# Optimization experiments

Hardware: AMD Instinct MI355X
Metric: run time of the kernel (lower is better)

## Reference

```python
import jax, jax.numpy as jnp
import numpy as np

DIM_Q = 1024
DIM_K = 1024
DIM_V = 1024


def setup_inputs() -> dict:
    key = jax.random.key(0)
    kx, kq, kk, kv = jax.random.split(key, 4)
    x = jax.random.normal(kx, (4, 2048, DIM_Q), dtype=jnp.float32)
    # torch nn.Linear weights: [out_features, in_features], y = x @ W.T
    scale = 1.0 / np.sqrt(DIM_Q)
    Wq = jax.random.uniform(kq, (DIM_K, DIM_Q), dtype=jnp.float32, minval=-scale, maxval=scale)
    Wk = jax.random.uniform(kk, (DIM_K, DIM_Q), dtype=jnp.float32, minval=-scale, maxval=scale)
    Wv = jax.random.uniform(kv, (DIM_V, DIM_Q), dtype=jnp.float32, minval=-scale, maxval=scale)
    return {"x": x, "Wq": Wq, "Wk": Wk, "Wv": Wv}


def reference(x, Wq, Wk, Wv):
    # q, k: [b, s, dim_k]; v: [b, s, dim_v]
    q = jnp.einsum('bsd,kd->bsk', x, Wq)
    k = jnp.einsum('bsd,kd->bsk', x, Wk)
    v = jnp.einsum('bsd,vd->bsv', x, Wv)
    norm_fact = 1.0 / jnp.sqrt(jnp.asarray(DIM_K, dtype=x.dtype))
    score = jnp.einsum('bik,bjk->bij', q, k) * norm_fact  # [b, s, s]
    score = jax.nn.softmax(score, axis=-1)
    att = jnp.einsum('bij,bjv->biv', score, v)
    att = att + v  # is_residual=True
    return att
```

## Files before the change

kernel.cpp:

```cpp
#include <hip/hip_runtime.h>
#include <hip/hip_bf16.h>

using bf16 = __hip_bfloat16;
typedef __attribute__((ext_vector_type(8))) short short8;
typedef __attribute__((ext_vector_type(4))) float floatx4;
typedef __attribute__((ext_vector_type(8))) int int8v;

__device__ __forceinline__ void async_ld16(const void* g, void* l) {
  __builtin_amdgcn_global_load_lds((const __attribute__((address_space(1))) void*)g,
                                   (__attribute__((address_space(3))) void*)l, 16, 0, 0);
}

__device__ __forceinline__ int pk4_fp8(float a, float b, float c, float d) {
  int v = __builtin_amdgcn_cvt_pk_fp8_f32(a, b, 0, false);
  return __builtin_amdgcn_cvt_pk_fp8_f32(c, d, v, true);
}

__device__ __forceinline__ int8v ld_frag16(const unsigned char* lo, const unsigned char* hi) {
  int4 l0 = *(const int4*)lo, h0 = *(const int4*)hi;
  int8v v;
  v[0] = l0.x; v[1] = l0.y; v[2] = l0.z; v[3] = l0.w;
  v[4] = h0.x; v[5] = h0.y; v[6] = h0.z; v[7] = h0.w;
  return v;
}


__device__ __forceinline__ void gemm_core(const bf16* __restrict__ At,
                                          const bf16* __restrict__ Bt,
                                          int K, bf16* lA, bf16* lB,
                                          floatx4 acc[4][4]) {
  const int tid  = threadIdx.x;
  const int w    = tid >> 6;
  const int lane = tid & 63;
  const int subM = (w >> 1) * 64;
  const int subN = (w & 1) * 64;
  const int fr   = lane & 15;
  const int fq   = lane >> 4;

  int srow[4], scol[4], sdst[4];
#pragma unroll
  for (int q = 0; q < 4; ++q) {
    int p = q * 256 + w * 64 + lane;
    int r = p >> 3;
    int j = (p & 7) ^ (r & 7);
    srow[q] = r;
    scol[q] = j * 8;
    sdst[q] = (q * 256 + w * 64) * 8;
  }
  int offA[2][4], offB[2][4];
#pragma unroll
  for (int kc = 0; kc < 2; ++kc)
#pragma unroll
    for (int i = 0; i < 4; ++i) {
      int rA = subM + i * 16 + fr;
      offA[kc][i] = (rA * 8 + ((kc * 4 + fq) ^ (rA & 7))) * 8;
      int rB = subN + i * 16 + fr;
      offB[kc][i] = (rB * 8 + ((kc * 4 + fq) ^ (rB & 7))) * 8;
    }

  floatx4 zero = {0.f, 0.f, 0.f, 0.f};
#pragma unroll
  for (int i = 0; i < 4; ++i)
#pragma unroll
    for (int j = 0; j < 4; ++j) acc[i][j] = zero;

  for (int k0 = 0; k0 < K; k0 += 64) {
    __syncthreads();
#pragma unroll
    for (int q = 0; q < 4; ++q) {
      async_ld16(At + (size_t)srow[q] * K + k0 + scol[q], lA + sdst[q]);
      async_ld16(Bt + (size_t)srow[q] * K + k0 + scol[q], lB + sdst[q]);
    }
    __syncthreads();
#pragma unroll
    for (int kc = 0; kc < 2; ++kc) {
      short8 a[4], b[4];
#pragma unroll
      for (int i = 0; i < 4; ++i) a[i] = *(const short8*)(lA + offA[kc][i]);
#pragma unroll
      for (int j = 0; j < 4; ++j) b[j] = *(const short8*)(lB + offB[kc][j]);
#pragma unroll
      for (int i = 0; i < 4; ++i)
#pragma unroll
        for (int j = 0; j < 4; ++j)
          acc[i][j] = __builtin_amdgcn_mfma_f32_16x16x32_bf16(a[i], b[j], acc[i][j], 0, 0, 0);
    }
  }
}

__device__ __forceinline__ void gemm_core_f8(const unsigned char* __restrict__ At,
                                             const unsigned char* __restrict__ Bt,
                                             int K, unsigned char* lA, unsigned char* lB,
                                             floatx4 acc[4][4]) {
  const int tid  = threadIdx.x;
  const int w    = tid >> 6;
  const int lane = tid & 63;
  const int subM = (w >> 1) * 64;
  const int subN = (w & 1) * 64;
  const int fr   = lane & 15;
  const int fq   = lane >> 4;

  int srow[4], scol[4], sdst[4];
#pragma unroll
  for (int q = 0; q < 4; ++q) {
    int p = q * 256 + w * 64 + lane;
    int r = p >> 3;
    int j = (p & 7) ^ (r & 7) ^ ((r & 8) >> 1);
    srow[q] = r;
    scol[q] = j * 16;
    sdst[q] = (q * 256 + w * 64) * 16;
  }
  int offA[2][4], offB[2][4];
#pragma unroll
  for (int h = 0; h < 2; ++h)
#pragma unroll
    for (int i = 0; i < 4; ++i) {
      int rA = subM + i * 16 + fr;
      offA[h][i] = rA * 128 + (((fq * 2 + h) ^ (rA & 7) ^ ((rA & 8) >> 1)) * 16);
      int rB = subN + i * 16 + fr;
      offB[h][i] = rB * 128 + (((fq * 2 + h) ^ (rB & 7) ^ ((rB & 8) >> 1)) * 16);
    }

  floatx4 zero = {0.f, 0.f, 0.f, 0.f};
#pragma unroll
  for (int i = 0; i < 4; ++i)
#pragma unroll
    for (int j = 0; j < 4; ++j) acc[i][j] = zero;

  for (int k0 = 0; k0 < K; k0 += 128) {
    __syncthreads();
#pragma unroll
    for (int q = 0; q < 4; ++q) {
      async_ld16(At + (size_t)srow[q] * K + k0 + scol[q], lA + sdst[q]);
      async_ld16(Bt + (size_t)srow[q] * K + k0 + scol[q], lB + sdst[q]);
    }
    __syncthreads();
    int8v a[4], b[4];
#pragma unroll
    for (int i = 0; i < 4; ++i) a[i] = ld_frag16(lA + offA[0][i], lA + offA[1][i]);
#pragma unroll
    for (int j = 0; j < 4; ++j) b[j] = ld_frag16(lB + offB[0][j], lB + offB[1][j]);
#pragma unroll
    for (int i = 0; i < 4; ++i)
#pragma unroll
      for (int j = 0; j < 4; ++j)
        acc[i][j] = __builtin_amdgcn_mfma_scale_f32_16x16x128_f8f6f4(
            a[i], b[j], acc[i][j], 0, 0, 0, 0x7F7F7F7F, 0, 0x7F7F7F7F);
  }
}

__device__ __forceinline__ void gemm_core_f8_v2(const unsigned char* __restrict__ At,
                                                const unsigned char* __restrict__ Bt,
                                                int K, unsigned char* lA, unsigned char* lB,
                                                floatx4 acc[4][8]) {
  const int tid  = threadIdx.x;
  const int w    = tid >> 6;
  const int lane = tid & 63;
  const int subM = (w >> 1) * 64;
  const int subN = (w & 1) * 128;
  const int fr   = lane & 15;
  const int fq   = lane >> 4;

  int srowA[4], scolA[4], sdstA[4];
#pragma unroll
  for (int q = 0; q < 4; ++q) {
    int p = q * 256 + w * 64 + lane;
    int r = p >> 3;
    int j = (p & 7) ^ (r & 7) ^ ((r & 8) >> 1);
    srowA[q] = r; scolA[q] = j * 16; sdstA[q] = (q * 256 + w * 64) * 16;
  }
  int srowB[8], scolB[8], sdstB[8];
#pragma unroll
  for (int q = 0; q < 8; ++q) {
    int p = q * 256 + w * 64 + lane;
    int r = p >> 3;
    int j = (p & 7) ^ (r & 7) ^ ((r & 8) >> 1);
    srowB[q] = r; scolB[q] = j * 16; sdstB[q] = (q * 256 + w * 64) * 16;
  }
  int offA[2][4], offB[2][8];
#pragma unroll
  for (int h = 0; h < 2; ++h) {
#pragma unroll
    for (int i = 0; i < 4; ++i) {
      int rA = subM + i * 16 + fr;
      offA[h][i] = rA * 128 + (((fq * 2 + h) ^ (rA & 7) ^ ((rA & 8) >> 1)) * 16);
    }
#pragma unroll
    for (int j = 0; j < 8; ++j) {
      int rB = subN + j * 16 + fr;
      offB[h][j] = rB * 128 + (((fq * 2 + h) ^ (rB & 7) ^ ((rB & 8) >> 1)) * 16);
    }
  }

  floatx4 zero = {0.f, 0.f, 0.f, 0.f};
#pragma unroll
  for (int i = 0; i < 4; ++i)
#pragma unroll
    for (int j = 0; j < 8; ++j) acc[i][j] = zero;

  for (int k0 = 0; k0 < K; k0 += 128) {
    __syncthreads();
#pragma unroll
    for (int q = 0; q < 4; ++q)
      async_ld16(At + (size_t)srowA[q] * K + k0 + scolA[q], lA + sdstA[q]);
#pragma unroll
    for (int q = 0; q < 8; ++q)
      async_ld16(Bt + (size_t)srowB[q] * K + k0 + scolB[q], lB + sdstB[q]);
    __syncthreads();
    int8v a[4];
#pragma unroll
    for (int i = 0; i < 4; ++i) a[i] = ld_frag16(lA + offA[0][i], lA + offA[1][i]);
#pragma unroll
    for (int j = 0; j < 8; ++j) {
      int8v bf = ld_frag16(lB + offB[0][j], lB + offB[1][j]);
#pragma unroll
      for (int i = 0; i < 4; ++i)
        acc[i][j] = __builtin_amdgcn_mfma_scale_f32_16x16x128_f8f6f4(
            a[i], bf, acc[i][j], 0, 0, 0, 0x7F7F7F7F, 0, 0x7F7F7F7F);
    }
  }
}

__global__ __launch_bounds__(256, 2) void proj_gemm(
    const bf16* __restrict__ Xbf, const bf16* __restrict__ Wvbf, bf16* __restrict__ Vbf,
    const unsigned char* __restrict__ X8, const unsigned char* __restrict__ Wq8,
    const unsigned char* __restrict__ Wk8,
    unsigned char* __restrict__ Qf8, unsigned char* __restrict__ Kf8) {
  __shared__ __align__(16) char lds[49152];
  const int id = blockIdx.x;
  const int tid = threadIdx.x, w = tid >> 6, lane = tid & 63;
  const int fr = lane & 15, fq = lane >> 4;

  if (id < 512) {
    const int r = id & 7, g = id >> 3;
    const int ty = r * 8 + (g & 7), tx = g >> 3;
    bf16* lA = (bf16*)lds;
    bf16* lB = (bf16*)(lds + 16384);
    floatx4 acc[4][4];
    gemm_core(Xbf + (size_t)ty * 128 * 1024, Wvbf + (size_t)tx * 128 * 1024,
              1024, lA, lB, acc);
    const int subM = (w >> 1) * 64, subN = (w & 1) * 64;
    const int rowBase = ty * 128 + subM;
    const int colBase = tx * 128 + subN;
#pragma unroll
    for (int i = 0; i < 4; ++i)
#pragma unroll
      for (int j = 0; j < 4; ++j)
#pragma unroll
        for (int rr = 0; rr < 4; ++rr) {
          int row = rowBase + i * 16 + fq * 4 + rr;
          int col = colBase + j * 16 + fr;
          Vbf[(size_t)row * 1024 + col] = __float2bfloat16(acc[i][j][rr]);
        }
  } else {
    const int local = id - 512;
    const int z = local >> 8, lid = local & 255;
    const int r = lid & 7, g = lid >> 3;
    const int ty = r * 8 + (g & 7);
    const int tx = g >> 3;
    unsigned char* lA = (unsigned char*)lds;
    unsigned char* lB = (unsigned char*)(lds + 16384);
    floatx4 acc[4][8];
    gemm_core_f8_v2(X8 + (size_t)ty * 128 * 1024,
                    (z == 0 ? Wq8 : Wk8) + (size_t)tx * 256 * 1024, 1024, lA, lB, acc);
    unsigned char* dst = (z == 0) ? Qf8 : Kf8;
    const int subM = (w >> 1) * 64, subN = (w & 1) * 128;
    const int rowBase = ty * 128 + subM;
    const int colBase = tx * 256 + subN;
#pragma unroll
    for (int i = 0; i < 4; ++i)
#pragma unroll
      for (int rr = 0; rr < 4; ++rr) {
        int row = rowBase + i * 16 + fq * 4 + rr;
        unsigned int p0 = (unsigned int)pk4_fp8(acc[i][0][rr], acc[i][1][rr],
                                                acc[i][2][rr], acc[i][3][rr]);
        unsigned int p1 = (unsigned int)pk4_fp8(acc[i][4][rr], acc[i][5][rr],
                                                acc[i][6][rr], acc[i][7][rr]);
        *(unsigned int*)&dst[(size_t)row * 1024 + colBase + fr * 4] = p0;
        *(unsigned int*)&dst[(size_t)row * 1024 + colBase + 64 + fr * 4] = p1;
      }
  }
}

__global__ __launch_bounds__(256, 2) void mid_kernel(
    const unsigned char* __restrict__ Qf8, const unsigned char* __restrict__ Kf8,
    unsigned char* __restrict__ S8, float* __restrict__ l,
    const bf16* __restrict__ Vbf, unsigned char* __restrict__ Vt8) {
  __shared__ __align__(16) char lds[49152];
  const int id = blockIdx.x;
  const int t = threadIdx.x;

  if (id < 512) {
    const int r = id & 7, g = id >> 3;
    const int b = g >> 4;
    const int rem = g & 15;
    const int ty = r * 2 + (rem & 1);
    const int tx = rem >> 1;
    unsigned char* lA = (unsigned char*)lds;
    unsigned char* lB = (unsigned char*)(lds + 16384);
    floatx4 acc[4][8];
    gemm_core_f8_v2(Qf8 + (size_t)b * 2048 * 1024 + (size_t)ty * 128 * 1024,
                    Kf8 + (size_t)b * 2048 * 1024 + (size_t)tx * 256 * 1024,
                    1024, lA, lB, acc);
    const int w = t >> 6, lane = t & 63;
    const int subM = (w >> 1) * 64, subN = (w & 1) * 128;
    const int fr = lane & 15, fq = lane >> 4;
    const int rowBase = ty * 128 + subM;
    const int colBase = tx * 256 + subN;
    unsigned char* Sb = S8 + (size_t)b * 2048 * 2048;
    float* lb = l + (size_t)b * 2048;
#pragma unroll
    for (int i = 0; i < 4; ++i)
#pragma unroll
      for (int rr = 0; rr < 4; ++rr) {
        int row = rowBase + i * 16 + fq * 4 + rr;
        unsigned int p0 = (unsigned int)pk4_fp8(
            __expf(acc[i][0][rr] * 0.03125f), __expf(acc[i][1][rr] * 0.03125f),
            __expf(acc[i][2][rr] * 0.03125f), __expf(acc[i][3][rr] * 0.03125f));
        unsigned int p1 = (unsigned int)pk4_fp8(
            __expf(acc[i][4][rr] * 0.03125f), __expf(acc[i][5][rr] * 0.03125f),
            __expf(acc[i][6][rr] * 0.03125f), __expf(acc[i][7][rr] * 0.03125f));
        *(unsigned int*)&Sb[(size_t)row * 2048 + colBase + fr * 4] = p0;
        *(unsigned int*)&Sb[(size_t)row * 2048 + colBase + 64 + fr * 4] = p1;
        float psum = __builtin_amdgcn_cvt_f32_fp8(p0, 0) + __builtin_amdgcn_cvt_f32_fp8(p0, 1) +
                     __builtin_amdgcn_cvt_f32_fp8(p0, 2) + __builtin_amdgcn_cvt_f32_fp8(p0, 3) +
                     __builtin_amdgcn_cvt_f32_fp8(p1, 0) + __builtin_amdgcn_cvt_f32_fp8(p1, 1) +
                     __builtin_amdgcn_cvt_f32_fp8(p1, 2) + __builtin_amdgcn_cvt_f32_fp8(p1, 3);
        psum += __shfl_xor(psum, 1, 64);
        psum += __shfl_xor(psum, 2, 64);
        psum += __shfl_xor(psum, 4, 64);
        psum += __shfl_xor(psum, 8, 64);
        if (fr == 0) atomicAdd(&lb[row], psum);
      }
  } else {
    const int t2 = id - 512;
    const int b = t2 >> 9, rem = t2 & 511;
    const int xs = rem & 31, yv = rem >> 5;
    const int s0 = xs * 64, v0 = yv * 64;
    short(*tile)[72] = (short(*)[72])lds;
#pragma unroll
    for (int i = 0; i < 2; ++i) {
      int c = t + i * 256;
      int row = c >> 3, cj = c & 7;
      *(short8*)&tile[row][cj * 8] =
          *(const short8*)&Vbf[((size_t)(b * 2048 + s0 + row)) * 1024 + v0 + cj * 8];
    }
    __syncthreads();
    const int vrow = t >> 2, sq = t & 3;
#pragma unroll
    for (int hc = 0; hc < 2; ++hc) {
      float f[8];
#pragma unroll
      for (int e = 0; e < 8; ++e) {
        int p = sq * 16 + hc * 8 + e;
        int s = (p & 3) * 16 + (p >> 2);
        short sh = tile[s][vrow];
        f[e] = __bfloat162float(*(bf16*)&sh);
      }
      uint2 packed;
      packed.x = (unsigned int)pk4_fp8(f[0], f[1], f[2], f[3]);
      packed.y = (unsigned int)pk4_fp8(f[4], f[5], f[6], f[7]);
      *(uint2*)&Vt8[((size_t)(b * 1024 + v0 + vrow)) * 2048 + s0 + sq * 16 + hc * 8] = packed;
    }
  }
}

__global__ __launch_bounds__(256) void pv_gemm(const unsigned char* __restrict__ S8,
                                               const unsigned char* __restrict__ Vt8,
                                               const bf16* __restrict__ Vbf,
                                               const float* __restrict__ l,
                                               float* __restrict__ out) {
  __shared__ __align__(16) char lds[32768];
  unsigned char* lA = (unsigned char*)lds;
  unsigned char* lB = (unsigned char*)(lds + 16384);
  const int id = blockIdx.x;
  const int r = id & 7, g = id >> 3;
  const int b = g >> 4;
  const int rem = g & 15;
  const int ty = r * 2 + (rem & 1);
  const int tx = rem >> 1;

  floatx4 acc[4][4];
  gemm_core_f8(S8 + (size_t)b * 2048 * 2048 + (size_t)ty * 128 * 2048,
               Vt8 + (size_t)b * 1024 * 2048 + (size_t)tx * 128 * 2048,
               2048, lA, lB, acc);

  const int tid = threadIdx.x, w = tid >> 6, lane = tid & 63;
  const int subM = (w >> 1) * 64, subN = (w & 1) * 64;
  const int fr = lane & 15, fq = lane >> 4;
  const int rowBase = ty * 128 + subM;
  const int colBase = tx * 128 + subN;
  const float* lb = l + (size_t)b * 2048;
#pragma unroll
  for (int i = 0; i < 4; ++i)
#pragma unroll
    for (int rr = 0; rr < 4; ++rr) {
      int row = rowBase + i * 16 + fq * 4 + rr;
      float inv = 1.0f / lb[row];
#pragma unroll
      for (int j = 0; j < 4; ++j) {
        int col = colBase + j * 16 + fr;
        size_t oi = ((size_t)b * 2048 + row) * 1024 + col;
        out[oi] = acc[i][j][rr] * inv + __bfloat162float(Vbf[oi]);
      }
    }
}

__global__ void cast_all(const float* __restrict__ x, const float* __restrict__ wq,
                         const float* __restrict__ wk, const float* __restrict__ wv,
                         bf16* __restrict__ Xbf, unsigned char* __restrict__ X8,
                         unsigned char* __restrict__ Wq8, unsigned char* __restrict__ Wk8,
                         bf16* __restrict__ Wvbf, float* __restrict__ l) {
  const int blk = blockIdx.x;
  const int t = threadIdx.x;
  if (blk < 8192) {
    int i = blk * 256 + t;
    float4 f = ((const float4*)x)[i];
    bf16 tmp[4] = {__float2bfloat16(f.x), __float2bfloat16(f.y),
                   __float2bfloat16(f.z), __float2bfloat16(f.w)};
    ((ushort4*)Xbf)[i] = *(const ushort4*)tmp;
    ((unsigned int*)X8)[i] = (unsigned int)pk4_fp8(f.x, f.y, f.z, f.w);
  } else if (blk < 10240) {
    const float* src = (blk < 9216) ? wq : wk;
    unsigned char* dst = (blk < 9216) ? Wq8 : Wk8;
    int i = ((blk - 8192) & 1023) * 256 + t;
    float4 f = ((const float4*)src)[i];
    ((unsigned int*)dst)[i] = (unsigned int)pk4_fp8(f.x, f.y, f.z, f.w);
  } else if (blk < 11264) {
    int i = (blk - 10240) * 256 + t;
    float4 f = ((const float4*)wv)[i];
    bf16 tmp[4] = {__float2bfloat16(f.x), __float2bfloat16(f.y),
                   __float2bfloat16(f.z), __float2bfloat16(f.w)};
    ((ushort4*)Wvbf)[i] = *(const ushort4*)tmp;
  } else {
    int i = (blk - 11264) * 256 + t;
    ((float4*)l)[i] = make_float4(0.f, 0.f, 0.f, 0.f);
  }
}

extern "C" void kernel_launch(void* const* d_in, const int* in_sizes, int n_in,
                              void* d_out, int out_size, void* d_ws, size_t ws_size,
                              hipStream_t stream) {
  const float* x  = (const float*)d_in[0];
  const float* Wq = (const float*)d_in[1];
  const float* Wk = (const float*)d_in[2];
  const float* Wv = (const float*)d_in[3];
  float* out = (float*)d_out;

  char* ws = (char*)d_ws;
  bf16* Xbf = (bf16*)ws;                   ws += (size_t)8192 * 1024 * 2;
  unsigned char* X8 = (unsigned char*)ws;  ws += (size_t)8192 * 1024;
  unsigned char* Wq8 = (unsigned char*)ws; ws += (size_t)1024 * 1024;
  unsigned char* Wk8 = (unsigned char*)ws; ws += (size_t)1024 * 1024;
  bf16* Wvbf = (bf16*)ws;                  ws += (size_t)1024 * 1024 * 2;
  unsigned char* Qf8 = (unsigned char*)ws; ws += (size_t)8192 * 1024;
  unsigned char* Kf8 = (unsigned char*)ws; ws += (size_t)8192 * 1024;
  bf16* Vbf = (bf16*)ws;                   ws += (size_t)8192 * 1024 * 2;
  unsigned char* Vt8 = (unsigned char*)ws; ws += (size_t)4 * 1024 * 2048;
  unsigned char* S8  = (unsigned char*)ws; ws += (size_t)4 * 2048 * 2048;
  float* l = (float*)ws;                   ws += (size_t)8192 * 4;

  cast_all<<<11272, 256, 0, stream>>>(x, Wq, Wk, Wv, Xbf, X8, Wq8, Wk8, Wvbf, l);
  proj_gemm<<<1024, 256, 0, stream>>>(Xbf, Wvbf, Vbf, X8, Wq8, Wk8, Qf8, Kf8);
  mid_kernel<<<2560, 256, 0, stream>>>(Qf8, Kf8, S8, l, Vbf, Vt8);
  pv_gemm<<<512, 256, 0, stream>>>(S8, Vt8, Vbf, l, out);
}
```

Measured before the change: 176.0 us.

## Fuse V transpose-to-fp8 into projection epilogue and coarsen cast kernel

The V projection epilogue now also packs its accumulators to fp8 and transposes them through a swizzled LDS tile, writing Vt8 directly. This removes the separate transpose blocks in mid_kernel that re-read Vbf from global memory. The cast kernel now processes four vectors per thread with fewer blocks, and pv_gemm gains a launch bound of two blocks per CU. The cost is extra epilogue work, including two barriers, in the V blocks of proj_gemm.

```diff
diff --git a/kernel.cpp b/kernel.cpp
--- a/kernel.cpp
+++ b/kernel.cpp
@@ -225,7 +225,8 @@
     const bf16* __restrict__ Xbf, const bf16* __restrict__ Wvbf, bf16* __restrict__ Vbf,
     const unsigned char* __restrict__ X8, const unsigned char* __restrict__ Wq8,
     const unsigned char* __restrict__ Wk8,
-    unsigned char* __restrict__ Qf8, unsigned char* __restrict__ Kf8) {
+    unsigned char* __restrict__ Qf8, unsigned char* __restrict__ Kf8,
+    unsigned char* __restrict__ Vt8) {
   __shared__ __align__(16) char lds[49152];
   const int id = blockIdx.x;
   const int tid = threadIdx.x, w = tid >> 6, lane = tid & 63;
@@ -252,6 +253,41 @@
           int col = colBase + j * 16 + fr;
           Vbf[(size_t)row * 1024 + col] = __float2bfloat16(acc[i][j][rr]);
         }
+
+    __syncthreads();
+    unsigned int* tp = (unsigned int*)lds;
+#pragma unroll
+    for (int i = 0; i < 4; ++i) {
+      int rw = (subM + i * 16 + fq * 4) >> 2;
+#pragma unroll
+      for (int j = 0; j < 4; ++j) {
+        int c = subN + j * 16 + fr;
+        tp[c * 32 + (rw ^ (c & 31))] =
+            (unsigned int)pk4_fp8(acc[i][j][0], acc[i][j][1], acc[i][j][2], acc[i][j][3]);
+      }
+    }
+    __syncthreads();
+    const int vrow = tid >> 1;
+    const int gh = tid & 1;
+    size_t ob = ((size_t)((ty >> 4) * 1024 + tx * 128 + vrow)) * 2048 +
+                (size_t)(ty & 15) * 128 + gh * 64;
+#pragma unroll
+    for (int h = 0; h < 4; ++h) {
+      unsigned int W0 = tp[vrow * 32 + ((gh * 16 + h) ^ (vrow & 31))];
+      unsigned int W1 = tp[vrow * 32 + ((gh * 16 + h + 4) ^ (vrow & 31))];
+      unsigned int W2 = tp[vrow * 32 + ((gh * 16 + h + 8) ^ (vrow & 31))];
+      unsigned int W3 = tp[vrow * 32 + ((gh * 16 + h + 12) ^ (vrow & 31))];
+      unsigned int t01l = __builtin_amdgcn_perm(W1, W0, 0x05010400u);
+      unsigned int t01h = __builtin_amdgcn_perm(W1, W0, 0x07030602u);
+      unsigned int t23l = __builtin_amdgcn_perm(W3, W2, 0x05010400u);
+      unsigned int t23h = __builtin_amdgcn_perm(W3, W2, 0x07030602u);
+      uint4 o;
+      o.x = __builtin_amdgcn_perm(t23l, t01l, 0x05040100u);
+      o.y = __builtin_amdgcn_perm(t23l, t01l, 0x07060302u);
+      o.z = __builtin_amdgcn_perm(t23h, t01h, 0x05040100u);
+      o.w = __builtin_amdgcn_perm(t23h, t01h, 0x07060302u);
+      *(uint4*)&Vt8[ob + h * 16] = o;
+    }
   } else {
     const int local = id - 512;
     const int z = local >> 8, lid = local & 255;
@@ -284,92 +320,59 @@
 
 __global__ __launch_bounds__(256, 2) void mid_kernel(
     const unsigned char* __restrict__ Qf8, const unsigned char* __restrict__ Kf8,
-    unsigned char* __restrict__ S8, float* __restrict__ l,
-    const bf16* __restrict__ Vbf, unsigned char* __restrict__ Vt8) {
+    unsigned char* __restrict__ S8, float* __restrict__ l) {
   __shared__ __align__(16) char lds[49152];
   const int id = blockIdx.x;
   const int t = threadIdx.x;
 
-  if (id < 512) {
-    const int r = id & 7, g = id >> 3;
-    const int b = g >> 4;
-    const int rem = g & 15;
-    const int ty = r * 2 + (rem & 1);
-    const int tx = rem >> 1;
-    unsigned char* lA = (unsigned char*)lds;
-    unsigned char* lB = (unsigned char*)(lds + 16384);
-    floatx4 acc[4][8];
-    gemm_core_f8_v2(Qf8 + (size_t)b * 2048 * 1024 + (size_t)ty * 128 * 1024,
-                    Kf8 + (size_t)b * 2048 * 1024 + (size_t)tx * 256 * 1024,
-                    1024, lA, lB, acc);
-    const int w = t >> 6, lane = t & 63;
-    const int subM = (w >> 1) * 64, subN = (w & 1) * 128;
-    const int fr = lane & 15, fq = lane >> 4;
-    const int rowBase = ty * 128 + subM;
-    const int colBase = tx * 256 + subN;
-    unsigned char* Sb = S8 + (size_t)b * 2048 * 2048;
-    float* lb = l + (size_t)b * 2048;
-#pragma unroll
-    for (int i = 0; i < 4; ++i)
-#pragma unroll
-      for (int rr = 0; rr < 4; ++rr) {
-        int row = rowBase + i * 16 + fq * 4 + rr;
-        unsigned int p0 = (unsigned int)pk4_fp8(
-            __expf(acc[i][0][rr] * 0.03125f), __expf(acc[i][1][rr] * 0.03125f),
-            __expf(acc[i][2][rr] * 0.03125f), __expf(acc[i][3][rr] * 0.03125f));
-        unsigned int p1 = (unsigned int)pk4_fp8(
-            __expf(acc[i][4][rr] * 0.03125f), __expf(acc[i][5][rr] * 0.03125f),
-            __expf(acc[i][6][rr] * 0.03125f), __expf(acc[i][7][rr] * 0.03125f));
-        *(unsigned int*)&Sb[(size_t)row * 2048 + colBase + fr * 4] = p0;
-        *(unsigned int*)&Sb[(size_t)row * 2048 + colBase + 64 + fr * 4] = p1;
-        float psum = __builtin_amdgcn_cvt_f32_fp8(p0, 0) + __builtin_amdgcn_cvt_f32_fp8(p0, 1) +
-                     __builtin_amdgcn_cvt_f32_fp8(p0, 2) + __builtin_amdgcn_cvt_f32_fp8(p0, 3) +
-                     __builtin_amdgcn_cvt_f32_fp8(p1, 0) + __builtin_amdgcn_cvt_f32_fp8(p1, 1) +
-                     __builtin_amdgcn_cvt_f32_fp8(p1, 2) + __builtin_amdgcn_cvt_f32_fp8(p1, 3);
-        psum += __shfl_xor(psum, 1, 64);
-        psum += __shfl_xor(psum, 2, 64);
-        psum += __shfl_xor(psum, 4, 64);
-        psum += __shfl_xor(psum, 8, 64);
-        if (fr == 0) atomicAdd(&lb[row], psum);
-      }
-  } else {
-    const int t2 = id - 512;
-    const int b = t2 >> 9, rem = t2 & 511;
-    const int xs = rem & 31, yv = rem >> 5;
-    const int s0 = xs * 64, v0 = yv * 64;
-    short(*tile)[72] = (short(*)[72])lds;
-#pragma unroll
-    for (int i = 0; i < 2; ++i) {
-      int c = t + i * 256;
-      int row = c >> 3, cj = c & 7;
-      *(short8*)&tile[row][cj * 8] =
-          *(const short8*)&Vbf[((size_t)(b * 2048 + s0 + row)) * 1024 + v0 + cj * 8];
-    }
-    __syncthreads();
-    const int vrow = t >> 2, sq = t & 3;
-#pragma unroll
-    for (int hc = 0; hc < 2; ++hc) {
-      float f[8];
-#pragma unroll
-      for (int e = 0; e < 8; ++e) {
-        int p = sq * 16 + hc * 8 + e;
-        int s = (p & 3) * 16 + (p >> 2);
-        short sh = tile[s][vrow];
-        f[e] = __bfloat162float(*(bf16*)&sh);
-      }
-      uint2 packed;
-      packed.x = (unsigned int)pk4_fp8(f[0], f[1], f[2], f[3]);
-      packed.y = (unsigned int)pk4_fp8(f[4], f[5], f[6], f[7]);
-      *(uint2*)&Vt8[((size_t)(b * 1024 + v0 + vrow)) * 2048 + s0 + sq * 16 + hc * 8] = packed;
-    }
-  }
-}
-
-__global__ __launch_bounds__(256) void pv_gemm(const unsigned char* __restrict__ S8,
-                                               const unsigned char* __restrict__ Vt8,
-                                               const bf16* __restrict__ Vbf,
-                                               const float* __restrict__ l,
-                                               float* __restrict__ out) {
+  const int r = id & 7, g = id >> 3;
+  const int b = g >> 4;
+  const int rem = g & 15;
+  const int ty = r * 2 + (rem & 1);
+  const int tx = rem >> 1;
+  unsigned char* lA = (unsigned char*)lds;
+  unsigned char* lB = (unsigned char*)(lds + 16384);
+  floatx4 acc[4][8];
+  gemm_core_f8_v2(Qf8 + (size_t)b * 2048 * 1024 + (size_t)ty * 128 * 1024,
+                  Kf8 + (size_t)b * 2048 * 1024 + (size_t)tx * 256 * 1024,
+                  1024, lA, lB, acc);
+  const int w = t >> 6, lane = t & 63;
+  const int subM = (w >> 1) * 64, subN = (w & 1) * 128;
+  const int fr = lane & 15, fq = lane >> 4;
+  const int rowBase = ty * 128 + subM;
+  const int colBase = tx * 256 + subN;
+  unsigned char* Sb = S8 + (size_t)b * 2048 * 2048;
+  float* lb = l + (size_t)b * 2048;
+#pragma unroll
+  for (int i = 0; i < 4; ++i)
+#pragma unroll
+    for (int rr = 0; rr < 4; ++rr) {
+      int row = rowBase + i * 16 + fq * 4 + rr;
+      unsigned int p0 = (unsigned int)pk4_fp8(
+          __expf(acc[i][0][rr] * 0.03125f), __expf(acc[i][1][rr] * 0.03125f),
+          __expf(acc[i][2][rr] * 0.03125f), __expf(acc[i][3][rr] * 0.03125f));
+      unsigned int p1 = (unsigned int)pk4_fp8(
+          __expf(acc[i][4][rr] * 0.03125f), __expf(acc[i][5][rr] * 0.03125f),
+          __expf(acc[i][6][rr] * 0.03125f), __expf(acc[i][7][rr] * 0.03125f));
+      *(unsigned int*)&Sb[(size_t)row * 2048 + colBase + fr * 4] = p0;
+      *(unsigned int*)&Sb[(size_t)row * 2048 + colBase + 64 + fr * 4] = p1;
+      float psum = __builtin_amdgcn_cvt_f32_fp8(p0, 0) + __builtin_amdgcn_cvt_f32_fp8(p0, 1) +
+                   __builtin_amdgcn_cvt_f32_fp8(p0, 2) + __builtin_amdgcn_cvt_f32_fp8(p0, 3) +
+                   __builtin_amdgcn_cvt_f32_fp8(p1, 0) + __builtin_amdgcn_cvt_f32_fp8(p1, 1) +
+                   __builtin_amdgcn_cvt_f32_fp8(p1, 2) + __builtin_amdgcn_cvt_f32_fp8(p1, 3);
+      psum += __shfl_xor(psum, 1, 64);
+      psum += __shfl_xor(psum, 2, 64);
+      psum += __shfl_xor(psum, 4, 64);
+      psum += __shfl_xor(psum, 8, 64);
+      if (fr == 0) atomicAdd(&lb[row], psum);
+    }
+}
+
+__global__ __launch_bounds__(256, 2) void pv_gemm(const unsigned char* __restrict__ S8,
+                                                  const unsigned char* __restrict__ Vt8,
+                                                  const bf16* __restrict__ Vbf,
+                                                  const float* __restrict__ l,
+                                                  float* __restrict__ out) {
   __shared__ __align__(16) char lds[32768];
   unsigned char* lA = (unsigned char*)lds;
   unsigned char* lB = (unsigned char*)(lds + 16384);
@@ -413,28 +416,39 @@
                          bf16* __restrict__ Wvbf, float* __restrict__ l) {
   const int blk = blockIdx.x;
   const int t = threadIdx.x;
-  if (blk < 8192) {
-    int i = blk * 256 + t;
-    float4 f = ((const float4*)x)[i];
-    bf16 tmp[4] = {__float2bfloat16(f.x), __float2bfloat16(f.y),
-                   __float2bfloat16(f.z), __float2bfloat16(f.w)};
-    ((ushort4*)Xbf)[i] = *(const ushort4*)tmp;
-    ((unsigned int*)X8)[i] = (unsigned int)pk4_fp8(f.x, f.y, f.z, f.w);
-  } else if (blk < 10240) {
-    const float* src = (blk < 9216) ? wq : wk;
-    unsigned char* dst = (blk < 9216) ? Wq8 : Wk8;
-    int i = ((blk - 8192) & 1023) * 256 + t;
-    float4 f = ((const float4*)src)[i];
-    ((unsigned int*)dst)[i] = (unsigned int)pk4_fp8(f.x, f.y, f.z, f.w);
-  } else if (blk < 11264) {
-    int i = (blk - 10240) * 256 + t;
-    float4 f = ((const float4*)wv)[i];
-    bf16 tmp[4] = {__float2bfloat16(f.x), __float2bfloat16(f.y),
-                   __float2bfloat16(f.z), __float2bfloat16(f.w)};
-    ((ushort4*)Wvbf)[i] = *(const ushort4*)tmp;
+  if (blk < 2048) {
+#pragma unroll
+    for (int k = 0; k < 4; ++k) {
+      int i = blk * 1024 + k * 256 + t;
+      float4 f = ((const float4*)x)[i];
+      bf16 tmp[4] = {__float2bfloat16(f.x), __float2bfloat16(f.y),
+                     __float2bfloat16(f.z), __float2bfloat16(f.w)};
+      ((ushort4*)Xbf)[i] = *(const ushort4*)tmp;
+      ((unsigned int*)X8)[i] = (unsigned int)pk4_fp8(f.x, f.y, f.z, f.w);
+    }
+  } else if (blk < 2560) {
+    const float* src = (blk < 2304) ? wq : wk;
+    unsigned char* dst = (blk < 2304) ? Wq8 : Wk8;
+    int base = ((blk - 2048) & 255) * 1024;
+#pragma unroll
+    for (int k = 0; k < 4; ++k) {
+      int i = base + k * 256 + t;
+      float4 f = ((const float4*)src)[i];
+      ((unsigned int*)dst)[i] = (unsigned int)pk4_fp8(f.x, f.y, f.z, f.w);
+    }
+  } else if (blk < 2816) {
+#pragma unroll
+    for (int k = 0; k < 4; ++k) {
+      int i = (blk - 2560) * 1024 + k * 256 + t;
+      float4 f = ((const float4*)wv)[i];
+      bf16 tmp[4] = {__float2bfloat16(f.x), __float2bfloat16(f.y),
+                     __float2bfloat16(f.z), __float2bfloat16(f.w)};
+      ((ushort4*)Wvbf)[i] = *(const ushort4*)tmp;
+    }
   } else {
-    int i = (blk - 11264) * 256 + t;
-    ((float4*)l)[i] = make_float4(0.f, 0.f, 0.f, 0.f);
+#pragma unroll
+    for (int k = 0; k < 8; ++k)
+      ((float4*)l)[k * 256 + t] = make_float4(0.f, 0.f, 0.f, 0.f);
   }
 }
 
@@ -460,8 +474,8 @@
   unsigned char* S8  = (unsigned char*)ws; ws += (size_t)4 * 2048 * 2048;
   float* l = (float*)ws;                   ws += (size_t)8192 * 4;
 
-  cast_all<<<11272, 256, 0, stream>>>(x, Wq, Wk, Wv, Xbf, X8, Wq8, Wk8, Wvbf, l);
-  proj_gemm<<<1024, 256, 0, stream>>>(Xbf, Wvbf, Vbf, X8, Wq8, Wk8, Qf8, Kf8);
-  mid_kernel<<<2560, 256, 0, stream>>>(Qf8, Kf8, S8, l, Vbf, Vt8);
+  cast_all<<<2817, 256, 0, stream>>>(x, Wq, Wk, Wv, Xbf, X8, Wq8, Wk8, Wvbf, l);
+  proj_gemm<<<1024, 256, 0, stream>>>(Xbf, Wvbf, Vbf, X8, Wq8, Wk8, Qf8, Kf8, Vt8);
+  mid_kernel<<<512, 256, 0, stream>>>(Qf8, Kf8, S8, l);
   pv_gemm<<<512, 256, 0, stream>>>(S8, Vt8, Vbf, l, out);
 }
```

Measured after the change: 179.7 us. +2.1%, slower.

## Double-buffer LDS in fp8 PV GEMM to overlap loads with MFMA

Applied to the files above, without the earlier changes.

Converts the fp8 PV GEMM core to a two-stage LDS ping-pong. The next K-tile is issued with async global-to-LDS loads while MFMAs run on the current tile, using vmcnt-based waits and raw barriers instead of two syncthreads per iteration. It also raises wave priority around the MFMA block and sets a launch bound of two blocks per CU. LDS use doubles to 64KB per block, which may limit occupancy, and the last iteration issues a redundant prefetch of tile 0.

```diff
diff --git a/kernel.cpp b/kernel.cpp
--- a/kernel.cpp
+++ b/kernel.cpp
@@ -88,10 +88,10 @@
   }
 }
 
-__device__ __forceinline__ void gemm_core_f8(const unsigned char* __restrict__ At,
-                                             const unsigned char* __restrict__ Bt,
-                                             int K, unsigned char* lA, unsigned char* lB,
-                                             floatx4 acc[4][4]) {
+__device__ __forceinline__ void gemm_core_f8_dbuf(const unsigned char* __restrict__ At,
+                                                  const unsigned char* __restrict__ Bt,
+                                                  int K, unsigned char* lds0,
+                                                  floatx4 acc[4][4]) {
   const int tid  = threadIdx.x;
   const int w    = tid >> 6;
   const int lane = tid & 63;
@@ -121,31 +121,50 @@
       offB[h][i] = rB * 128 + (((fq * 2 + h) ^ (rB & 7) ^ ((rB & 8) >> 1)) * 16);
     }
 
+  auto stage = [&](int buf, int k0) {
+    unsigned char* base = lds0 + buf * 32768;
+#pragma unroll
+    for (int q = 0; q < 4; ++q) {
+      async_ld16(At + (size_t)srow[q] * K + k0 + scol[q], base + sdst[q]);
+      async_ld16(Bt + (size_t)srow[q] * K + k0 + scol[q], base + 16384 + sdst[q]);
+    }
+  };
+
   floatx4 zero = {0.f, 0.f, 0.f, 0.f};
 #pragma unroll
   for (int i = 0; i < 4; ++i)
 #pragma unroll
     for (int j = 0; j < 4; ++j) acc[i][j] = zero;
 
-  for (int k0 = 0; k0 < K; k0 += 128) {
-    __syncthreads();
-#pragma unroll
-    for (int q = 0; q < 4; ++q) {
-      async_ld16(At + (size_t)srow[q] * K + k0 + scol[q], lA + sdst[q]);
-      async_ld16(Bt + (size_t)srow[q] * K + k0 + scol[q], lB + sdst[q]);
-    }
-    __syncthreads();
+  const int nt = K >> 7;
+  stage(0, 0);
+  asm volatile("s_waitcnt vmcnt(0)" ::: "memory");
+  __builtin_amdgcn_s_barrier();
+
+  for (int t = 0; t < nt; ++t) {
+    const int nb = (t + 1) & 1;
+    const int tn = (t + 1 < nt) ? (t + 1) : 0;
+    stage(nb, tn << 7);
+    asm volatile("s_waitcnt vmcnt(8)" ::: "memory");
+    __builtin_amdgcn_s_barrier();
+    __builtin_amdgcn_sched_barrier(0);
+
+    const unsigned char* lA = lds0 + (t & 1) * 32768;
+    const unsigned char* lB = lA + 16384;
     int8v a[4], b[4];
 #pragma unroll
     for (int i = 0; i < 4; ++i) a[i] = ld_frag16(lA + offA[0][i], lA + offA[1][i]);
 #pragma unroll
     for (int j = 0; j < 4; ++j) b[j] = ld_frag16(lB + offB[0][j], lB + offB[1][j]);
+    __builtin_amdgcn_s_setprio(1);
 #pragma unroll
     for (int i = 0; i < 4; ++i)
 #pragma unroll
       for (int j = 0; j < 4; ++j)
         acc[i][j] = __builtin_amdgcn_mfma_scale_f32_16x16x128_f8f6f4(
             a[i], b[j], acc[i][j], 0, 0, 0, 0x7F7F7F7F, 0, 0x7F7F7F7F);
+    __builtin_amdgcn_s_setprio(0);
+    __builtin_amdgcn_s_barrier();
   }
 }
 
@@ -365,14 +384,12 @@
   }
 }
 
-__global__ __launch_bounds__(256) void pv_gemm(const unsigned char* __restrict__ S8,
-                                               const unsigned char* __restrict__ Vt8,
-                                               const bf16* __restrict__ Vbf,
-                                               const float* __restrict__ l,
-                                               float* __restrict__ out) {
-  __shared__ __align__(16) char lds[32768];
-  unsigned char* lA = (unsigned char*)lds;
-  unsigned char* lB = (unsigned char*)(lds + 16384);
+__global__ __launch_bounds__(256, 2) void pv_gemm(const unsigned char* __restrict__ S8,
+                                                  const unsigned char* __restrict__ Vt8,
+                                                  const bf16* __restrict__ Vbf,
+                                                  const float* __restrict__ l,
+                                                  float* __restrict__ out) {
+  __shared__ __align__(16) char lds[65536];
   const int id = blockIdx.x;
   const int r = id & 7, g = id >> 3;
   const int b = g >> 4;
@@ -381,9 +398,9 @@
   const int tx = rem >> 1;
 
   floatx4 acc[4][4];
-  gemm_core_f8(S8 + (size_t)b * 2048 * 2048 + (size_t)ty * 128 * 2048,
-               Vt8 + (size_t)b * 1024 * 2048 + (size_t)tx * 128 * 2048,
-               2048, lA, lB, acc);
+  gemm_core_f8_dbuf(S8 + (size_t)b * 2048 * 2048 + (size_t)ty * 128 * 2048,
+                    Vt8 + (size_t)b * 1024 * 2048 + (size_t)tx * 128 * 2048,
+                    2048, (unsigned char*)lds, acc);
 
   const int tid = threadIdx.x, w = tid >> 6, lane = tid & 63;
   const int subM = (w >> 1) * 64, subN = (w & 1) * 64;
```

Measured after the change: 176.8 us. About the same (+0.5%).
